# Performance work log

Measured on AMD Instinct MI355X. Metric: run time of the kernel, lower is better.

The kernel has to match this reference:

```python
import jax, jax.numpy as jnp
import numpy as np


def _bilinear_sample(img, gx, gy):
    """torch.nn.functional.grid_sample equivalent: bilinear, padding_mode='zeros',
    align_corners=True. img: [H,W]; gx,gy: normalized coords in [-1,1] (x->width, y->height)."""
    H, W = img.shape
    x = (gx + 1.0) * 0.5 * (W - 1)
    y = (gy + 1.0) * 0.5 * (H - 1)
    x0 = jnp.floor(x)
    y0 = jnp.floor(y)
    x1 = x0 + 1.0
    y1 = y0 + 1.0
    wx1 = x - x0
    wx0 = 1.0 - wx1
    wy1 = y - y0
    wy0 = 1.0 - wy1

    def gather(xi, yi):
        valid = (xi >= 0) & (xi <= W - 1) & (yi >= 0) & (yi <= H - 1)
        xc = jnp.clip(xi, 0, W - 1).astype(jnp.int32)
        yc = jnp.clip(yi, 0, H - 1).astype(jnp.int32)
        return jnp.where(valid, img[yc, xc], jnp.zeros((), img.dtype))

    return (gather(x0, y0) * wx0 * wy0 + gather(x1, y0) * wx1 * wy0 +
            gather(x0, y1) * wx0 * wy1 + gather(x1, y1) * wx1 * wy1)


def _radon_forward(img, n_angles, det_count, image_size, step_size, sampling_points):
    distance = 2.0 / image_size
    # detector shifts [D]
    sx = jnp.linspace(-1.0, 1.0, det_count) * (det_count / 2.0) * distance * step_size
    sy = -np.sqrt(2.0).astype(np.float32)
    ey = -sy
    angles = jnp.linspace(0.0, np.pi, n_angles)[:, None] + np.pi / 2.0  # [A,1]
    ca, sa = jnp.cos(angles), jnp.sin(angles)
    rsx = sx * ca - sy * sa            # [A,D] ray start x
    rsy = sx * sa + sy * ca            # [A,D] ray start y
    rdx = (sx * ca + sy * sa) - rsx    # rex - rsx  (ex=sx, ey=+sqrt2 => ex*ca - ey*sa)
    # careful: rex = ex*cos - ey*sin = sx*ca - ey*sa = sx*ca + sy*sa (since ey=-sy)
    rdy = (sx * sa - sy * ca) - rsy    # rey = ex*sin + ey*cos = sx*sa - sy*ca
    S = sampling_points
    t = (jnp.arange(S, dtype=jnp.float32) / S)[:, None, None]  # [S,1,1]
    gx = rsx[None] + t * rdx[None]     # [S,A,D]
    gy = rsy[None] + t * rdy[None]
    samples = _bilinear_sample(img, gx, gy)        # [S,A,D]
    intens = jnp.sum(samples, axis=0) / S          # [A,D]
    # torch.rot90(out, 2) on [A*D,1] then view(A,D) == flip both axes of [A,D]
    return jnp.flip(intens, (0, 1))


def setup_inputs() -> dict:
    key = jax.random.key(0)
    img = jax.random.uniform(key, (512, 512), dtype=jnp.float32)
    return {
        "input": img,
        "n_angles": 512,
        "det_count": 512,
        "image_size": 512,
        "step_size": 1,
        "sampling_points": 256,
    }


def reference(input, n_angles, det_count, image_size, step_size, sampling_points):
    return _radon_forward(input, n_angles, det_count, image_size, step_size, sampling_points)
```

## Files before the change

kernel.cpp:

```cpp
#include <hip/hip_runtime.h>
#include <math.h>

#define IMG 512
#define A_N 512
#define D_N 512
#define S_N 256
#define PAD 8
#define PW  528

struct H4 { _Float16 v00, dx0, v01, dx1; };

__device__ __forceinline__ float imz(const float* __restrict__ im, int y, int x) {
    return ((unsigned)y < 512u && (unsigned)x < 512u) ? im[(y << 9) + x] : 0.0f;
}

__global__ __launch_bounds__(256)
void pack_fp16(const float* __restrict__ im,
               H4* __restrict__ pack, H4* __restrict__ packT) {
    __shared__ H4 ldsT[32][33];
    const int bx = blockIdx.x % 17, by = blockIdx.x / 17;
    const int tx = threadIdx.x & 31, ty0 = threadIdx.x >> 5;
    const int p = bx * 32 + tx;
    const int x = p - PAD;
    #pragma unroll
    for (int i = 0; i < 4; ++i) {
        const int ty = ty0 + i * 8;
        const int q = by * 32 + ty;
        const int y = q - PAD;
        const float a = imz(im, y, x);
        const float b = imz(im, y, x + 1);
        const float c = imz(im, y + 1, x);
        const float d = imz(im, y + 1, x + 1);
        if (p < PW && q < PW) {
            H4 e; e.v00 = (_Float16)a; e.dx0 = (_Float16)(b - a);
                  e.v01 = (_Float16)c; e.dx1 = (_Float16)(d - c);
            pack[q * PW + p] = e;
        }
        H4 eT; eT.v00 = (_Float16)a; eT.dx0 = (_Float16)(c - a);
               eT.v01 = (_Float16)b; eT.dx1 = (_Float16)(d - b);
        ldsT[tx][ty] = eT;
    }
    __syncthreads();
    #pragma unroll
    for (int i = 0; i < 4; ++i) {
        const int r  = ty0 + i * 8;
        const int qT = bx * 32 + r;
        const int pT = by * 32 + tx;
        if (qT < PW && pT < PW)
            packT[qT * PW + pT] = ldsT[r][tx];
    }
}

struct Samp { H4 P; float fx, fy; };

__device__ __forceinline__ Samp samp_load(const H4* __restrict__ base,
                                          float Ax, float Ay,
                                          float dBx, float dBy, int s) {
    Samp r;
    const float x = fmaf((float)s, dBx, Ax);
    const float y = fmaf((float)s, dBy, Ay);
    const int ix = (int)x, iy = (int)y;
    r.P  = base[iy * PW + ix];
    r.fx = x - (float)ix;
    r.fy = y - (float)iy;
    return r;
}

__device__ __forceinline__ void samp_acc(const Samp& r, float& acc) {
    const float t_ = fmaf(r.fx, (float)r.P.dx0, (float)r.P.v00);
    const float b_ = fmaf(r.fx, (float)r.P.dx1, (float)r.P.v01);
    acc = fmaf(r.fy, b_ - t_, t_ + acc);
}

__global__ __launch_bounds__(256, 6)
void radon_fp16(const H4* __restrict__ pack, const H4* __restrict__ packT,
                float* __restrict__ out) {
    const int blk  = blockIdx.x;
    const int a    = ((blk & 7) << 6) | ((blk >> 3) & 63);
    const int dg   = (int)((0x70615243u >> ((blk >> 9) * 4)) & 7u);
    const int w    = threadIdx.x >> 6;
    const int lane = threadIdx.x & 63;
    const int di   = lane & 15;
    const int js   = lane >> 4;
    const int d    = dg * 64 + w * 16 + di;

    const float PI  = 3.14159265358979323846f;
    const float SQ2 = 1.41421356237309504880f;

    const float ang = fmaf((float)a, PI / 511.0f, PI * 0.5f);
    float sa, ca;
    sincosf(ang, &sa, &ca);

    const float sx = fmaf((float)d, 2.0f / 511.0f, -1.0f);
    float Ax = (fmaf(sx, ca,  SQ2 * sa) + 1.0f) * 255.5f;
    float Ay = (fmaf(sx, sa, -SQ2 * ca) + 1.0f) * 255.5f;
    float Bx = -2.0f * SQ2 * sa * 255.5f;
    float By =  2.0f * SQ2 * ca * 255.5f;

    const H4* base = pack;
    if (fabsf(sa) > fabsf(ca)) {
        float t;
        t = Ax; Ax = Ay; Ay = t;
        t = Bx; Bx = By; By = t;
        base = packT;
    }

    float t0 = 0.0f, t1 = 255.0f / 256.0f;
    bool ok = true;
    {
        const float ra = (-1.0f - Ax) / Bx, rb = (512.0f - Ax) / Bx;
        t0 = fmaxf(t0, fminf(ra, rb));
        t1 = fminf(t1, fmaxf(ra, rb));
    }
    if (fabsf(By) > 1e-9f) {
        const float ra = (-1.0f - Ay) / By, rb = (512.0f - Ay) / By;
        t0 = fmaxf(t0, fminf(ra, rb));
        t1 = fminf(t1, fmaxf(ra, rb));
    } else if (Ay < -1.0f || Ay > 512.0f) ok = false;

    float acc0 = 0.0f, acc1 = 0.0f, acc2 = 0.0f, acc3 = 0.0f;
    if (ok && t0 <= t1) {
        const int s0  = max(0, (int)(t0 * 256.0f) - 1);
        const int s1  = min(S_N - 1, (int)(t1 * 256.0f) + 1);
        const int m   = s1 - (s0 + js);
        const int nk  = (m >= 0) ? ((m >> 2) + 1) : 0;

        const float dBx = Bx * (1.0f / 256.0f);
        const float dBy = By * (1.0f / 256.0f);
        Ax += (float)PAD;
        Ay += (float)PAD;

        int s = s0 + js;
        int k = 0;
        const int nFull = nk >> 2;
        if (nFull > 0) {
            Samp c0 = samp_load(base, Ax, Ay, dBx, dBy, s);
            Samp c1 = samp_load(base, Ax, Ay, dBx, dBy, s + 4);
            Samp c2 = samp_load(base, Ax, Ay, dBx, dBy, s + 8);
            Samp c3 = samp_load(base, Ax, Ay, dBx, dBy, s + 12);
            for (int g = 1; g < nFull; ++g) {
                Samp n0 = samp_load(base, Ax, Ay, dBx, dBy, s + 16);
                Samp n1 = samp_load(base, Ax, Ay, dBx, dBy, s + 20);
                Samp n2 = samp_load(base, Ax, Ay, dBx, dBy, s + 24);
                Samp n3 = samp_load(base, Ax, Ay, dBx, dBy, s + 28);
                samp_acc(c0, acc0);
                samp_acc(c1, acc1);
                samp_acc(c2, acc2);
                samp_acc(c3, acc3);
                c0 = n0; c1 = n1; c2 = n2; c3 = n3;
                s += 16;
            }
            samp_acc(c0, acc0);
            samp_acc(c1, acc1);
            samp_acc(c2, acc2);
            samp_acc(c3, acc3);
            s += 16;
            k = nFull << 2;
        }
        for (; k < nk; ++k, s += 4) {
            Samp r = samp_load(base, Ax, Ay, dBx, dBy, s);
            samp_acc(r, acc0);
        }
    }
    float acc = (acc0 + acc1) + (acc2 + acc3);

    acc += __shfl_xor(acc, 16);
    acc += __shfl_xor(acc, 32);

    __shared__ float red[64];
    if (lane < 16) red[w * 16 + di] = acc;
    __syncthreads();
    if (threadIdx.x < 64) {
        const float v = red[threadIdx.x] * (1.0f / 256.0f);
        const int dd = dg * 64 + threadIdx.x;
        out[(511 - a) * 512 + (511 - dd)] = v;
    }
}

__global__ __launch_bounds__(256)
void radon_direct(const float* __restrict__ img, float* __restrict__ out) {
    const int tid = blockIdx.x * 256 + threadIdx.x;
    const int d = tid & (D_N - 1);
    const int a = tid >> 9;
    const float PI  = 3.14159265358979323846f;
    const float SQ2 = 1.41421356237309504880f;
    const float ang = fmaf((float)a, PI / 511.0f, PI * 0.5f);
    float sa, ca;
    sincosf(ang, &sa, &ca);
    const float sx = fmaf((float)d, 2.0f / 511.0f, -1.0f);
    const float Ax = (fmaf(sx, ca,  SQ2 * sa) + 1.0f) * 255.5f;
    const float Ay = (fmaf(sx, sa, -SQ2 * ca) + 1.0f) * 255.5f;
    const float Bx = -2.0f * SQ2 * sa * 255.5f;
    const float By =  2.0f * SQ2 * ca * 255.5f;
    float acc = 0.0f;
    for (int s = 0; s < S_N; ++s) {
        const float t = (float)s * (1.0f / 256.0f);
        const float x = fmaf(t, Bx, Ax);
        const float y = fmaf(t, By, Ay);
        const float xf = floorf(x), yf = floorf(y);
        const float fx = x - xf, fy = y - yf;
        const int ix = (int)xf, iy = (int)yf;
        float wx0 = 1.0f - fx, wx1 = fx, wy0 = 1.0f - fy, wy1 = fy;
        wx0 = ((unsigned)ix       < 512u) ? wx0 : 0.0f;
        wx1 = ((unsigned)(ix + 1) < 512u) ? wx1 : 0.0f;
        wy0 = ((unsigned)iy       < 512u) ? wy0 : 0.0f;
        wy1 = ((unsigned)(iy + 1) < 512u) ? wy1 : 0.0f;
        const int ix0 = min(max(ix, 0), 511), ix1 = min(max(ix + 1, 0), 511);
        const int iy0 = min(max(iy, 0), 511), iy1 = min(max(iy + 1, 0), 511);
        const float* r0 = img + (iy0 << 9);
        const float* r1 = img + (iy1 << 9);
        acc = fmaf(fmaf(r0[ix1], wx1, r0[ix0] * wx0), wy0, acc);
        acc = fmaf(fmaf(r1[ix1], wx1, r1[ix0] * wx0), wy1, acc);
    }
    out[(511 - a) * 512 + (511 - d)] = acc * (1.0f / 256.0f);
}

extern "C" void kernel_launch(void* const* d_in, const int* in_sizes, int n_in,
                              void* d_out, int out_size, void* d_ws, size_t ws_size,
                              hipStream_t stream) {
    const float* img = (const float*)d_in[0];
    float* out = (float*)d_out;
    const size_t packBytes = (size_t)PW * PW * sizeof(H4);

    if (ws_size >= 2 * packBytes) {
        H4* pack  = (H4*)d_ws;
        H4* packT = pack + (size_t)PW * PW;
        pack_fp16<<<17 * 17, 256, 0, stream>>>(img, pack, packT);
        radon_fp16<<<4096, 256, 0, stream>>>(pack, packT, out);
    } else {
        radon_direct<<<(A_N * D_N) / 256, 256, 0, stream>>>(img, out);
    }
}
```

Measured before the change: 123.2 us.

## Split each ray's samples across blocks and combine partial sums with atomics

Work is redistributed so that each block loops over all 512 detectors of one angle, eight groups of 64 at a time, and covers only one of four contiguous quarter-ranges of each ray's clipped sample interval. Partial sums are added into the output with float atomicAdd, which needs a new zero-fill kernel first. Ray setup is hoisted and uses reciprocals, and the occupancy hint goes from 6 to 8 blocks. The aim is better load balance across rays of different lengths and less redundant per-ray setup. The cost is an extra launch, atomic traffic, and a summation order that is no longer deterministic.

```diff
diff --git a/kernel.cpp b/kernel.cpp
--- a/kernel.cpp
+++ b/kernel.cpp
@@ -12,6 +12,11 @@
 
 __device__ __forceinline__ float imz(const float* __restrict__ im, int y, int x) {
     return ((unsigned)y < 512u && (unsigned)x < 512u) ? im[(y << 9) + x] : 0.0f;
+}
+
+__global__ __launch_bounds__(256)
+void zero_out(float* __restrict__ out) {
+    out[blockIdx.x * 256 + threadIdx.x] = 0.0f;
 }
 
 __global__ __launch_bounds__(256)
@@ -72,17 +77,16 @@
     acc = fmaf(r.fy, b_ - t_, t_ + acc);
 }
 
-__global__ __launch_bounds__(256, 6)
+__global__ __launch_bounds__(256, 8)
 void radon_fp16(const H4* __restrict__ pack, const H4* __restrict__ packT,
                 float* __restrict__ out) {
     const int blk  = blockIdx.x;
     const int a    = ((blk & 7) << 6) | ((blk >> 3) & 63);
-    const int dg   = (int)((0x70615243u >> ((blk >> 9) * 4)) & 7u);
+    const int j    = (blk >> 9) & 3;
     const int w    = threadIdx.x >> 6;
     const int lane = threadIdx.x & 63;
     const int di   = lane & 15;
     const int js   = lane >> 4;
-    const int d    = dg * 64 + w * 16 + di;
 
     const float PI  = 3.14159265358979323846f;
     const float SQ2 = 1.41421356237309504880f;
@@ -91,89 +95,89 @@
     float sa, ca;
     sincosf(ang, &sa, &ca);
 
-    const float sx = fmaf((float)d, 2.0f / 511.0f, -1.0f);
-    float Ax = (fmaf(sx, ca,  SQ2 * sa) + 1.0f) * 255.5f;
-    float Ay = (fmaf(sx, sa, -SQ2 * ca) + 1.0f) * 255.5f;
+    float ux = ca, uy = sa;
+    float cx = fmaf(fmaf(SQ2, sa, 1.0f), 255.5f, (float)PAD);
+    float cy = fmaf(fmaf(-SQ2, ca, 1.0f), 255.5f, (float)PAD);
     float Bx = -2.0f * SQ2 * sa * 255.5f;
     float By =  2.0f * SQ2 * ca * 255.5f;
 
     const H4* base = pack;
     if (fabsf(sa) > fabsf(ca)) {
         float t;
-        t = Ax; Ax = Ay; Ay = t;
+        t = ux; ux = uy; uy = t;
+        t = cx; cx = cy; cy = t;
         t = Bx; Bx = By; By = t;
         base = packT;
     }
-
-    float t0 = 0.0f, t1 = 255.0f / 256.0f;
-    bool ok = true;
-    {
-        const float ra = (-1.0f - Ax) / Bx, rb = (512.0f - Ax) / Bx;
+    const float rBx = 1.0f / Bx, rBy = 1.0f / By;
+    const float dBx = Bx * (1.0f / 256.0f);
+    const float dBy = By * (1.0f / 256.0f);
+    const float XLO = (float)PAD - 1.0f;
+    const float XHI = (float)PAD + 512.0f;
+
+    #pragma unroll 1
+    for (int i = 0; i < 8; ++i) {
+        const int c  = i * 4 + w;
+        const int dd = 16 * c + di;
+        const float df = (float)dd - 255.5f;
+        const float Ax = fmaf(df, ux, cx);
+        const float Ay = fmaf(df, uy, cy);
+
+        float ra = (XLO - Ax) * rBx, rb = (XHI - Ax) * rBx;
+        float t0 = fmaxf(0.0f, fminf(ra, rb));
+        float t1 = fminf(255.0f / 256.0f, fmaxf(ra, rb));
+        ra = (XLO - Ay) * rBy; rb = (XHI - Ay) * rBy;
         t0 = fmaxf(t0, fminf(ra, rb));
         t1 = fminf(t1, fmaxf(ra, rb));
-    }
-    if (fabsf(By) > 1e-9f) {
-        const float ra = (-1.0f - Ay) / By, rb = (512.0f - Ay) / By;
-        t0 = fmaxf(t0, fminf(ra, rb));
-        t1 = fminf(t1, fmaxf(ra, rb));
-    } else if (Ay < -1.0f || Ay > 512.0f) ok = false;
-
-    float acc0 = 0.0f, acc1 = 0.0f, acc2 = 0.0f, acc3 = 0.0f;
-    if (ok && t0 <= t1) {
-        const int s0  = max(0, (int)(t0 * 256.0f) - 1);
-        const int s1  = min(S_N - 1, (int)(t1 * 256.0f) + 1);
-        const int m   = s1 - (s0 + js);
-        const int nk  = (m >= 0) ? ((m >> 2) + 1) : 0;
-
-        const float dBx = Bx * (1.0f / 256.0f);
-        const float dBy = By * (1.0f / 256.0f);
-        Ax += (float)PAD;
-        Ay += (float)PAD;
-
-        int s = s0 + js;
-        int k = 0;
-        const int nFull = nk >> 2;
-        if (nFull > 0) {
-            Samp c0 = samp_load(base, Ax, Ay, dBx, dBy, s);
-            Samp c1 = samp_load(base, Ax, Ay, dBx, dBy, s + 4);
-            Samp c2 = samp_load(base, Ax, Ay, dBx, dBy, s + 8);
-            Samp c3 = samp_load(base, Ax, Ay, dBx, dBy, s + 12);
-            for (int g = 1; g < nFull; ++g) {
-                Samp n0 = samp_load(base, Ax, Ay, dBx, dBy, s + 16);
-                Samp n1 = samp_load(base, Ax, Ay, dBx, dBy, s + 20);
-                Samp n2 = samp_load(base, Ax, Ay, dBx, dBy, s + 24);
-                Samp n3 = samp_load(base, Ax, Ay, dBx, dBy, s + 28);
+
+        float acc0 = 0.0f, acc1 = 0.0f, acc2 = 0.0f, acc3 = 0.0f;
+        if (t0 <= t1) {
+            const int s0 = max(0, (int)(t0 * 256.0f) - 1);
+            const int s1 = min(S_N - 1, (int)(t1 * 256.0f) + 1);
+            const int qn  = (s1 - s0 + 4) >> 2;
+            const int ws0 = s0 + j * qn;
+            const int ws1 = min(ws0 + qn - 1, s1);
+            const int m   = ws1 - (ws0 + js);
+            const int nk  = (m >= 0) ? ((m >> 2) + 1) : 0;
+
+            int s = ws0 + js;
+            int k = 0;
+            const int nFull = nk >> 2;
+            if (nFull > 0) {
+                Samp c0 = samp_load(base, Ax, Ay, dBx, dBy, s);
+                Samp c1 = samp_load(base, Ax, Ay, dBx, dBy, s + 4);
+                Samp c2 = samp_load(base, Ax, Ay, dBx, dBy, s + 8);
+                Samp c3 = samp_load(base, Ax, Ay, dBx, dBy, s + 12);
+                for (int g = 1; g < nFull; ++g) {
+                    Samp n0 = samp_load(base, Ax, Ay, dBx, dBy, s + 16);
+                    Samp n1 = samp_load(base, Ax, Ay, dBx, dBy, s + 20);
+                    Samp n2 = samp_load(base, Ax, Ay, dBx, dBy, s + 24);
+                    Samp n3 = samp_load(base, Ax, Ay, dBx, dBy, s + 28);
+                    samp_acc(c0, acc0);
+                    samp_acc(c1, acc1);
+                    samp_acc(c2, acc2);
+                    samp_acc(c3, acc3);
+                    c0 = n0; c1 = n1; c2 = n2; c3 = n3;
+                    s += 16;
+                }
                 samp_acc(c0, acc0);
                 samp_acc(c1, acc1);
                 samp_acc(c2, acc2);
                 samp_acc(c3, acc3);
-                c0 = n0; c1 = n1; c2 = n2; c3 = n3;
                 s += 16;
+                k = nFull << 2;
             }
-            samp_acc(c0, acc0);
-            samp_acc(c1, acc1);
-            samp_acc(c2, acc2);
-            samp_acc(c3, acc3);
-            s += 16;
-            k = nFull << 2;
+            for (; k < nk; ++k, s += 4) {
+                Samp r = samp_load(base, Ax, Ay, dBx, dBy, s);
+                samp_acc(r, acc0);
+            }
         }
-        for (; k < nk; ++k, s += 4) {
-            Samp r = samp_load(base, Ax, Ay, dBx, dBy, s);
-            samp_acc(r, acc0);
-        }
-    }
-    float acc = (acc0 + acc1) + (acc2 + acc3);
-
-    acc += __shfl_xor(acc, 16);
-    acc += __shfl_xor(acc, 32);
-
-    __shared__ float red[64];
-    if (lane < 16) red[w * 16 + di] = acc;
-    __syncthreads();
-    if (threadIdx.x < 64) {
-        const float v = red[threadIdx.x] * (1.0f / 256.0f);
-        const int dd = dg * 64 + threadIdx.x;
-        out[(511 - a) * 512 + (511 - dd)] = v;
+        float acc = (acc0 + acc1) + (acc2 + acc3);
+
+        acc += __shfl_xor(acc, 16);
+        acc += __shfl_xor(acc, 32);
+        if (lane < 16)
+            atomicAdd(&out[(511 - a) * 512 + (511 - dd)], acc * (1.0f / 256.0f));
     }
 }
 
@@ -226,7 +230,8 @@
         H4* pack  = (H4*)d_ws;
         H4* packT = pack + (size_t)PW * PW;
         pack_fp16<<<17 * 17, 256, 0, stream>>>(img, pack, packT);
-        radon_fp16<<<4096, 256, 0, stream>>>(pack, packT, out);
+        zero_out<<<(A_N * D_N) / 256, 256, 0, stream>>>(out);
+        radon_fp16<<<2048, 256, 0, stream>>>(pack, packT, out);
     } else {
         radon_direct<<<(A_N * D_N) / 256, 256, 0, stream>>>(img, out);
     }
```

Result: slower. 143.2 us (+16.2%).
